# Kernel optimization log

Measured on AMD Instinct MI355X. Metric: run time of the kernel, lower is better.

Reference implementation:

```python
import jax, jax.numpy as jnp
import numpy as np


def setup_inputs() -> dict:
    key = jax.random.key(0)
    k1, k2 = jax.random.split(key)
    N, P, D = 65536, 512, 256
    feature_vectors = jax.random.normal(k1, (N, D), dtype=jnp.float32)
    prototypes = jax.random.normal(k2, (P, D), dtype=jnp.float32)
    return {"feature_vectors": feature_vectors, "prototypes": prototypes}


def reference(feature_vectors, prototypes):
    # squared norms
    feat_sq = jnp.sum(feature_vectors * feature_vectors, axis=1)   # [N]
    proto_sq = jnp.sum(prototypes * prototypes, axis=1)            # [P]
    # cross term: [N, P]
    cross = feature_vectors @ prototypes.T
    # dists_to_protos: [N, P] = |f|^2 + |p|^2 - 2 f.p
    dists_to_protos = feat_sq[:, None] + proto_sq[None, :] - 2.0 * cross
    # dists_to_latents: [P, N] (original does a second matmul; it's the transpose)
    dists_to_latents = proto_sq[:, None] + feat_sq[None, :] - 2.0 * cross.T
    return (dists_to_protos, dists_to_latents)
```

## Files before the change

### kernel.cpp

```cpp
#include <hip/hip_runtime.h>
#include <hip/hip_bf16.h>


#define DD 256
#define PP 512
#define BN 64
#define TP 36

typedef short bf16x8 __attribute__((ext_vector_type(8)));
typedef float f32x16 __attribute__((ext_vector_type(16)));
typedef float f32x4 __attribute__((ext_vector_type(4)));
typedef unsigned short u16x4 __attribute__((ext_vector_type(4)));

__device__ __forceinline__ unsigned short f2bf(float f) {
    unsigned int u = __builtin_bit_cast(unsigned int, f);
    u = (u + 0x7fffu + ((u >> 16) & 1u)) >> 16;
    return (unsigned short)u;
}

__global__ __launch_bounds__(256) void proto_prep(const float* __restrict__ proto,
                                                  unsigned short* __restrict__ bw,
                                                  float* __restrict__ psq) {
    const int w = threadIdx.x >> 6, lane = threadIdx.x & 63;
    const int row = blockIdx.x * 4 + w;
    const f32x4 f = *(const f32x4*)(proto + (size_t)row * DD + lane * 4);
    u16x4 u;
    u.x = f2bf(f.x); u.y = f2bf(f.y); u.z = f2bf(f.z); u.w = f2bf(f.w);
    *(u16x4*)(bw + (size_t)row * DD + lane * 4) = u;
    float part = f.x * f.x + f.y * f.y + f.z * f.z + f.w * f.w;
    for (int o = 32; o > 0; o >>= 1) part += __shfl_xor(part, o, 64);
    if (lane == 0) psq[row] = part;
}

__global__ __launch_bounds__(512, 4) void proto_dist(
        const float* __restrict__ feat,
        const unsigned short* __restrict__ bw,
        const float* __restrict__ psq,
        float* __restrict__ out0,
        float* __restrict__ out1,
        int N) {
    __shared__ unsigned char S[8 * 32 * TP * 4];
    __shared__ float fsq[BN];
    unsigned short* A_lds = (unsigned short*)S;

    const int tid = threadIdx.x;
    const int w = tid >> 6, lane = tid & 63;
    const int n0 = blockIdx.x * BN;

    #pragma unroll
    for (int i = 0; i < 8; ++i) {
        const int row = i * 8 + w;
        const f32x4 f = __builtin_nontemporal_load(
            (const f32x4*)(feat + (size_t)(n0 + row) * DD + lane * 4));
        u16x4 u;
        u.x = f2bf(f.x); u.y = f2bf(f.y); u.z = f2bf(f.z); u.w = f2bf(f.w);
        *(u16x4*)&A_lds[row * 264 + lane * 4] = u;
        float part = f.x * f.x + f.y * f.y + f.z * f.z + f.w * f.w;
        for (int o = 32; o > 0; o >>= 1) part += __shfl_xor(part, o, 64);
        if (lane == 0) fsq[row] = part;
    }
    __syncthreads();

    const int r = w & 1;
    const int g = w >> 1;
    const int colbase = g * 128;
    const int l31 = lane & 31;
    const int hi = lane >> 5;

    f32x16 acc[4];
    #pragma unroll
    for (int t = 0; t < 4; ++t)
        #pragma unroll
        for (int e = 0; e < 16; ++e) acc[t][e] = 0.0f;

    const unsigned short* arow = &A_lds[(32 * r + l31) * 264 + hi * 8];
    const unsigned short* bbase = bw + (size_t)(colbase + l31) * DD + hi * 8;

    #pragma unroll 2
    for (int k0 = 0; k0 < DD; k0 += 16) {
        const bf16x8 a = *(const bf16x8*)(arow + k0);
        #pragma unroll
        for (int t = 0; t < 4; ++t) {
            const bf16x8 b = *(const bf16x8*)(bbase + (size_t)(32 * t) * DD + k0);
            acc[t] = __builtin_amdgcn_mfma_f32_32x32x16_bf16(a, b, acc[t], 0, 0, 0);
        }
    }

    __syncthreads();
    float* trans = ((float*)S) + w * (32 * TP);

    float fsq_q[4][4];
    #pragma unroll
    for (int q = 0; q < 4; ++q)
        #pragma unroll
        for (int e = 0; e < 4; ++e)
            fsq_q[q][e] = fsq[32 * r + e + 8 * q + 4 * hi];

    float* out0_base = out0 + (size_t)(n0 + 32 * r) * PP;

    #pragma unroll
    for (int t = 0; t < 4; ++t) {
        const int p = colbase + 32 * t + l31;
        const float psq_v = psq[p];
        #pragma unroll
        for (int q = 0; q < 4; ++q) {
            f32x4 d;
            #pragma unroll
            for (int e = 0; e < 4; ++e) {
                const int reg = 4 * q + e;
                const int n_l = e + 8 * q + 4 * hi;
                const float dist = fsq_q[q][e] + psq_v - 2.0f * acc[t][reg];
                d[e] = dist;
                __builtin_nontemporal_store(dist, out0_base + (size_t)n_l * PP + p);
            }
            *(f32x4*)&trans[l31 * TP + 8 * q + 4 * hi] = d;
        }
        #pragma unroll
        for (int j = 0; j < 4; ++j) {
            const int p_row = j * 8 + (lane >> 3);
            const int n_off = (lane & 7) * 4;
            const f32x4 v = *(const f32x4*)&trans[p_row * TP + n_off];
            __builtin_nontemporal_store(v,
                (f32x4*)(out1 + (size_t)(colbase + 32 * t + p_row) * N
                               + (n0 + 32 * r + n_off)));
        }
    }
}

extern "C" void kernel_launch(void* const* d_in, const int* in_sizes, int n_in,
                              void* d_out, int out_size, void* d_ws, size_t ws_size,
                              hipStream_t stream) {
    const float* feat = (const float*)d_in[0];
    const float* proto = (const float*)d_in[1];
    const int N = in_sizes[0] / DD;

    unsigned short* bw = (unsigned short*)d_ws;
    float* psq = (float*)((char*)d_ws + (size_t)PP * DD * 2);

    float* out0 = (float*)d_out;
    float* out1 = out0 + (size_t)N * PP;

    proto_prep<<<PP / 4, 256, 0, stream>>>(proto, bw, psq);
    proto_dist<<<N / BN, 512, 0, stream>>>(feat, bw, psq, out0, out1, N);
}
```

Measured before the change: 357.3 us.

## Load features straight from global into MFMA operands, dropping the LDS staging

The block tile shrinks from 64 to 32 feature rows with 4 waves instead of 8. Each wave now reads its fp32 feature slice from global memory inside the k-loop, converts it to bf16 in registers and accumulates the squared norm, with a lane shuffle replacing the shared fsq array. This removes the LDS staging pass and one barrier, and gives more, smaller blocks. In exchange, every wave in a block re-reads the same feature rows from global/cache (4x redundancy), and the strided per-lane loads are less coalesced.

After: 385.3 us. 7.8% more time.

```diff
diff --git a/kernel.cpp b/kernel.cpp
--- a/kernel.cpp
+++ b/kernel.cpp
@@ -4,7 +4,7 @@
 
 #define DD 256
 #define PP 512
-#define BN 64
+#define BN 32
 #define TP 36
 
 typedef short bf16x8 __attribute__((ext_vector_type(8)));
@@ -32,40 +32,24 @@
     if (lane == 0) psq[row] = part;
 }
 
-__global__ __launch_bounds__(512, 4) void proto_dist(
+__global__ __launch_bounds__(256, 4) void proto_dist(
         const float* __restrict__ feat,
         const unsigned short* __restrict__ bw,
         const float* __restrict__ psq,
         float* __restrict__ out0,
         float* __restrict__ out1,
         int N) {
-    __shared__ unsigned char S[8 * 32 * TP * 4];
-    __shared__ float fsq[BN];
-    unsigned short* A_lds = (unsigned short*)S;
+    __shared__ float S[4 * 32 * TP];
 
     const int tid = threadIdx.x;
     const int w = tid >> 6, lane = tid & 63;
     const int n0 = blockIdx.x * BN;
-
-    #pragma unroll
-    for (int i = 0; i < 8; ++i) {
-        const int row = i * 8 + w;
-        const f32x4 f = __builtin_nontemporal_load(
-            (const f32x4*)(feat + (size_t)(n0 + row) * DD + lane * 4));
-        u16x4 u;
-        u.x = f2bf(f.x); u.y = f2bf(f.y); u.z = f2bf(f.z); u.w = f2bf(f.w);
-        *(u16x4*)&A_lds[row * 264 + lane * 4] = u;
-        float part = f.x * f.x + f.y * f.y + f.z * f.z + f.w * f.w;
-        for (int o = 32; o > 0; o >>= 1) part += __shfl_xor(part, o, 64);
-        if (lane == 0) fsq[row] = part;
-    }
-    __syncthreads();
-
-    const int r = w & 1;
-    const int g = w >> 1;
-    const int colbase = g * 128;
+    const int colbase = w * 128;
     const int l31 = lane & 31;
     const int hi = lane >> 5;
+
+    const float* arow = feat + (size_t)(n0 + l31) * DD + hi * 8;
+    const unsigned short* bbase = bw + (size_t)(colbase + l31) * DD + hi * 8;
 
     f32x16 acc[4];
     #pragma unroll
@@ -73,12 +57,19 @@
         #pragma unroll
         for (int e = 0; e < 16; ++e) acc[t][e] = 0.0f;
 
-    const unsigned short* arow = &A_lds[(32 * r + l31) * 264 + hi * 8];
-    const unsigned short* bbase = bw + (size_t)(colbase + l31) * DD + hi * 8;
+    float part = 0.0f;
 
     #pragma unroll 2
     for (int k0 = 0; k0 < DD; k0 += 16) {
-        const bf16x8 a = *(const bf16x8*)(arow + k0);
+        const f32x4 f0 = *(const f32x4*)(arow + k0);
+        const f32x4 f1 = *(const f32x4*)(arow + k0 + 4);
+        bf16x8 a;
+        a[0] = (short)f2bf(f0.x); a[1] = (short)f2bf(f0.y);
+        a[2] = (short)f2bf(f0.z); a[3] = (short)f2bf(f0.w);
+        a[4] = (short)f2bf(f1.x); a[5] = (short)f2bf(f1.y);
+        a[6] = (short)f2bf(f1.z); a[7] = (short)f2bf(f1.w);
+        part += f0.x * f0.x + f0.y * f0.y + f0.z * f0.z + f0.w * f0.w
+              + f1.x * f1.x + f1.y * f1.y + f1.z * f1.z + f1.w * f1.w;
         #pragma unroll
         for (int t = 0; t < 4; ++t) {
             const bf16x8 b = *(const bf16x8*)(bbase + (size_t)(32 * t) * DD + k0);
@@ -86,17 +77,16 @@
         }
     }
 
-    __syncthreads();
-    float* trans = ((float*)S) + w * (32 * TP);
-
+    part += __shfl_xor(part, 32, 64);
     float fsq_q[4][4];
     #pragma unroll
     for (int q = 0; q < 4; ++q)
         #pragma unroll
         for (int e = 0; e < 4; ++e)
-            fsq_q[q][e] = fsq[32 * r + e + 8 * q + 4 * hi];
+            fsq_q[q][e] = __shfl(part, e + 8 * q + 4 * hi, 64);
 
-    float* out0_base = out0 + (size_t)(n0 + 32 * r) * PP;
+    float* trans = S + w * (32 * TP);
+    float* out0_base = out0 + (size_t)n0 * PP;
 
     #pragma unroll
     for (int t = 0; t < 4; ++t) {
@@ -122,7 +112,7 @@
             const f32x4 v = *(const f32x4*)&trans[p_row * TP + n_off];
             __builtin_nontemporal_store(v,
                 (f32x4*)(out1 + (size_t)(colbase + 32 * t + p_row) * N
-                               + (n0 + 32 * r + n_off)));
+                               + (n0 + n_off)));
         }
     }
 }
@@ -141,5 +131,5 @@
     float* out1 = out0 + (size_t)N * PP;
 
     proto_prep<<<PP / 4, 256, 0, stream>>>(proto, bw, psq);
-    proto_dist<<<N / BN, 512, 0, stream>>>(feat, bw, psq, out0, out1, N);
+    proto_dist<<<N / BN, 256, 0, stream>>>(feat, bw, psq, out0, out1, N);
 }
```

## Compute transposed output via second swapped MFMA instead of LDS transpose

Applied to the files above, without the earlier changes.

Replaces the LDS-based transpose of the cross-term tile with a second MFMA that uses swapped operands, so the transposed tile for the second output comes straight out of the accumulators. The block tile shrinks to 32 feature rows with 256 threads, and each wave loops over its four 32-column prototype tiles with fresh accumulators. This removes the shared-memory round trip and a barrier, but doubles the MFMA work. The second output is now written as scalar stores of 32 consecutive floats per row (128 bytes) rather than f32x4 vector stores. Prototype fragments are reread from global memory by twice as many blocks.

After: 376.0 us. 5.2% more time.

```diff
diff --git a/kernel.cpp b/kernel.cpp
--- a/kernel.cpp
+++ b/kernel.cpp
@@ -4,8 +4,8 @@
 
 #define DD 256
 #define PP 512
-#define BN 64
-#define TP 36
+#define BN 32
+#define AP 280
 
 typedef short bf16x8 __attribute__((ext_vector_type(8)));
 typedef float f32x16 __attribute__((ext_vector_type(16)));
@@ -32,16 +32,15 @@
     if (lane == 0) psq[row] = part;
 }
 
-__global__ __launch_bounds__(512, 4) void proto_dist(
+__global__ __launch_bounds__(256, 4) void proto_dist(
         const float* __restrict__ feat,
         const unsigned short* __restrict__ bw,
         const float* __restrict__ psq,
         float* __restrict__ out0,
         float* __restrict__ out1,
         int N) {
-    __shared__ unsigned char S[8 * 32 * TP * 4];
+    __shared__ unsigned short A_lds[BN * AP];
     __shared__ float fsq[BN];
-    unsigned short* A_lds = (unsigned short*)S;
 
     const int tid = threadIdx.x;
     const int w = tid >> 6, lane = tid & 63;
@@ -49,80 +48,69 @@
 
     #pragma unroll
     for (int i = 0; i < 8; ++i) {
-        const int row = i * 8 + w;
+        const int row = i * 4 + w;
         const f32x4 f = __builtin_nontemporal_load(
             (const f32x4*)(feat + (size_t)(n0 + row) * DD + lane * 4));
         u16x4 u;
         u.x = f2bf(f.x); u.y = f2bf(f.y); u.z = f2bf(f.z); u.w = f2bf(f.w);
-        *(u16x4*)&A_lds[row * 264 + lane * 4] = u;
+        *(u16x4*)&A_lds[row * AP + lane * 4] = u;
         float part = f.x * f.x + f.y * f.y + f.z * f.z + f.w * f.w;
         for (int o = 32; o > 0; o >>= 1) part += __shfl_xor(part, o, 64);
         if (lane == 0) fsq[row] = part;
     }
     __syncthreads();
 
-    const int r = w & 1;
-    const int g = w >> 1;
-    const int colbase = g * 128;
     const int l31 = lane & 31;
     const int hi = lane >> 5;
+    const int colT = w * 128;
 
-    f32x16 acc[4];
-    #pragma unroll
-    for (int t = 0; t < 4; ++t)
-        #pragma unroll
-        for (int e = 0; e < 16; ++e) acc[t][e] = 0.0f;
+    const unsigned short* arow = &A_lds[l31 * AP + hi * 8];
 
-    const unsigned short* arow = &A_lds[(32 * r + l31) * 264 + hi * 8];
-    const unsigned short* bbase = bw + (size_t)(colbase + l31) * DD + hi * 8;
-
-    #pragma unroll 2
-    for (int k0 = 0; k0 < DD; k0 += 16) {
-        const bf16x8 a = *(const bf16x8*)(arow + k0);
-        #pragma unroll
-        for (int t = 0; t < 4; ++t) {
-            const bf16x8 b = *(const bf16x8*)(bbase + (size_t)(32 * t) * DD + k0);
-            acc[t] = __builtin_amdgcn_mfma_f32_32x32x16_bf16(a, b, acc[t], 0, 0, 0);
-        }
-    }
-
-    __syncthreads();
-    float* trans = ((float*)S) + w * (32 * TP);
-
-    float fsq_q[4][4];
+    f32x4 fsq_q[4];
     #pragma unroll
     for (int q = 0; q < 4; ++q)
-        #pragma unroll
-        for (int e = 0; e < 4; ++e)
-            fsq_q[q][e] = fsq[32 * r + e + 8 * q + 4 * hi];
-
-    float* out0_base = out0 + (size_t)(n0 + 32 * r) * PP;
+        fsq_q[q] = *(const f32x4*)&fsq[8 * q + 4 * hi];
+    const float fsq_lane = fsq[l31];
 
     #pragma unroll
     for (int t = 0; t < 4; ++t) {
-        const int p = colbase + 32 * t + l31;
-        const float psq_v = psq[p];
+        const int pbase = colT + 32 * t;
+        const unsigned short* bb = bw + (size_t)(pbase + l31) * DD + hi * 8;
+
+        f32x16 acc, acc2;
+        #pragma unroll
+        for (int e = 0; e < 16; ++e) { acc[e] = 0.0f; acc2[e] = 0.0f; }
+
+        #pragma unroll 4
+        for (int k0 = 0; k0 < DD; k0 += 16) {
+            const bf16x8 a = *(const bf16x8*)(arow + k0);
+            const bf16x8 b = *(const bf16x8*)(bb + k0);
+            acc  = __builtin_amdgcn_mfma_f32_32x32x16_bf16(a, b, acc,  0, 0, 0);
+            acc2 = __builtin_amdgcn_mfma_f32_32x32x16_bf16(b, a, acc2, 0, 0, 0);
+        }
+
+        const float psq_lane = psq[pbase + l31];
+        float* o0 = out0 + (size_t)n0 * PP + pbase + l31;
         #pragma unroll
         for (int q = 0; q < 4; ++q) {
-            f32x4 d;
             #pragma unroll
             for (int e = 0; e < 4; ++e) {
-                const int reg = 4 * q + e;
                 const int n_l = e + 8 * q + 4 * hi;
-                const float dist = fsq_q[q][e] + psq_v - 2.0f * acc[t][reg];
-                d[e] = dist;
-                __builtin_nontemporal_store(dist, out0_base + (size_t)n_l * PP + p);
+                const float dist = fsq_q[q][e] + psq_lane - 2.0f * acc[4 * q + e];
+                __builtin_nontemporal_store(dist, o0 + (size_t)n_l * PP);
             }
-            *(f32x4*)&trans[l31 * TP + 8 * q + 4 * hi] = d;
         }
+
+        float* o1 = out1 + (size_t)pbase * N + n0 + l31;
         #pragma unroll
-        for (int j = 0; j < 4; ++j) {
-            const int p_row = j * 8 + (lane >> 3);
-            const int n_off = (lane & 7) * 4;
-            const f32x4 v = *(const f32x4*)&trans[p_row * TP + n_off];
-            __builtin_nontemporal_store(v,
-                (f32x4*)(out1 + (size_t)(colbase + 32 * t + p_row) * N
-                               + (n0 + 32 * r + n_off)));
+        for (int q = 0; q < 4; ++q) {
+            const f32x4 ps4 = *(const f32x4*)(psq + pbase + 8 * q + 4 * hi);
+            #pragma unroll
+            for (int e = 0; e < 4; ++e) {
+                const int p_l = e + 8 * q + 4 * hi;
+                const float dist = fsq_lane + ps4[e] - 2.0f * acc2[4 * q + e];
+                __builtin_nontemporal_store(dist, o1 + (size_t)p_l * N);
+            }
         }
     }
 }
@@ -141,5 +129,5 @@
     float* out1 = out0 + (size_t)N * PP;
 
     proto_prep<<<PP / 4, 256, 0, stream>>>(proto, bw, psq);
-    proto_dist<<<N / BN, 512, 0, stream>>>(feat, bw, psq, out0, out1, N);
+    proto_dist<<<N / BN, 256, 0, stream>>>(feat, bw, psq, out0, out1, N);
 }
```

## Stage both outputs through block-wide LDS tiles for fully coalesced vector stores

Applied to the files above, without the earlier changes.

Replaces the per-wave scalar out0 stores and the 32-wide transposed out1 stores with block-wide staging. Each output is written in phases: 32 rows x 512 columns for out0, and 128 prototypes x 64 features for out1, each followed by 16-byte nontemporal stores of whole contiguous rows. The goal is to remove uncoalesced scalar writes to out0 and short segments to out1 on this store-bound kernel. In exchange, LDS grows to 64KB, which limits occupancy, and it adds about ten block barriers that serialise waves during the epilogue.

After: 359.2 us. Within noise of the previous version (+0.5%).

```diff
diff --git a/kernel.cpp b/kernel.cpp
--- a/kernel.cpp
+++ b/kernel.cpp
@@ -5,7 +5,8 @@
 #define DD 256
 #define PP 512
 #define BN 64
-#define TP 36
+#define AP 280
+#define O1S 68
 
 typedef short bf16x8 __attribute__((ext_vector_type(8)));
 typedef float f32x16 __attribute__((ext_vector_type(16)));
@@ -39,9 +40,10 @@
         float* __restrict__ out0,
         float* __restrict__ out1,
         int N) {
-    __shared__ unsigned char S[8 * 32 * TP * 4];
+    __shared__ unsigned char S[65536];
     __shared__ float fsq[BN];
     unsigned short* A_lds = (unsigned short*)S;
+    float* lds_f = (float*)S;
 
     const int tid = threadIdx.x;
     const int w = tid >> 6, lane = tid & 63;
@@ -54,7 +56,7 @@
             (const f32x4*)(feat + (size_t)(n0 + row) * DD + lane * 4));
         u16x4 u;
         u.x = f2bf(f.x); u.y = f2bf(f.y); u.z = f2bf(f.z); u.w = f2bf(f.w);
-        *(u16x4*)&A_lds[row * 264 + lane * 4] = u;
+        *(u16x4*)&A_lds[row * AP + lane * 4] = u;
         float part = f.x * f.x + f.y * f.y + f.z * f.z + f.w * f.w;
         for (int o = 32; o > 0; o >>= 1) part += __shfl_xor(part, o, 64);
         if (lane == 0) fsq[row] = part;
@@ -63,9 +65,11 @@
 
     const int r = w & 1;
     const int g = w >> 1;
-    const int colbase = g * 128;
+    const int colT = g * 128;
     const int l31 = lane & 31;
     const int hi = lane >> 5;
+
+    const unsigned short* arow = &A_lds[(32 * r + l31) * AP + hi * 8];
 
     f32x16 acc[4];
     #pragma unroll
@@ -73,57 +77,81 @@
         #pragma unroll
         for (int e = 0; e < 16; ++e) acc[t][e] = 0.0f;
 
-    const unsigned short* arow = &A_lds[(32 * r + l31) * 264 + hi * 8];
-    const unsigned short* bbase = bw + (size_t)(colbase + l31) * DD + hi * 8;
-
     #pragma unroll 2
     for (int k0 = 0; k0 < DD; k0 += 16) {
         const bf16x8 a = *(const bf16x8*)(arow + k0);
         #pragma unroll
         for (int t = 0; t < 4; ++t) {
-            const bf16x8 b = *(const bf16x8*)(bbase + (size_t)(32 * t) * DD + k0);
+            const bf16x8 b = *(const bf16x8*)(
+                bw + (size_t)(colT + 32 * t + l31) * DD + hi * 8 + k0);
             acc[t] = __builtin_amdgcn_mfma_f32_32x32x16_bf16(a, b, acc[t], 0, 0, 0);
         }
     }
 
-    __syncthreads();
-    float* trans = ((float*)S) + w * (32 * TP);
-
-    float fsq_q[4][4];
+    f32x4 fsq_q[4];
     #pragma unroll
     for (int q = 0; q < 4; ++q)
-        #pragma unroll
-        for (int e = 0; e < 4; ++e)
-            fsq_q[q][e] = fsq[32 * r + e + 8 * q + 4 * hi];
+        fsq_q[q] = *(const f32x4*)&fsq[32 * r + 8 * q + 4 * hi];
+    f32x4 psqv;
+    #pragma unroll
+    for (int t = 0; t < 4; ++t) psqv[t] = psq[colT + 32 * t + l31];
 
-    float* out0_base = out0 + (size_t)(n0 + 32 * r) * PP;
+    __syncthreads();
 
     #pragma unroll
-    for (int t = 0; t < 4; ++t) {
-        const int p = colbase + 32 * t + l31;
-        const float psq_v = psq[p];
+    for (int s = 0; s < 2; ++s) {
+        if (r == s) {
+            #pragma unroll
+            for (int t = 0; t < 4; ++t)
+                #pragma unroll
+                for (int q = 0; q < 4; ++q)
+                    #pragma unroll
+                    for (int e = 0; e < 4; ++e) {
+                        const int n_l = e + 8 * q + 4 * hi;
+                        lds_f[n_l * 512 + colT + 32 * t + l31] =
+                            fsq_q[q][e] + psqv[t] - 2.0f * acc[t][4 * q + e];
+                    }
+        }
+        __syncthreads();
+        float* o0 = out0 + (size_t)(n0 + 32 * s) * PP;
+        const int row = tid >> 7;
+        const int off = (tid & 127) * 4;
         #pragma unroll
-        for (int q = 0; q < 4; ++q) {
-            f32x4 d;
+        for (int rr = 0; rr < 8; ++rr) {
+            const f32x4 v = *(const f32x4*)&lds_f[(row + 4 * rr) * 512 + off];
+            __builtin_nontemporal_store(
+                v, (f32x4*)(o0 + (size_t)(row + 4 * rr) * PP + off));
+        }
+        __syncthreads();
+    }
+
+    #pragma unroll
+    for (int sp = 0; sp < 4; ++sp) {
+        if (g == sp) {
             #pragma unroll
-            for (int e = 0; e < 4; ++e) {
-                const int reg = 4 * q + e;
-                const int n_l = e + 8 * q + 4 * hi;
-                const float dist = fsq_q[q][e] + psq_v - 2.0f * acc[t][reg];
-                d[e] = dist;
-                __builtin_nontemporal_store(dist, out0_base + (size_t)n_l * PP + p);
+            for (int t = 0; t < 4; ++t) {
+                const int p_loc = 32 * t + l31;
+                #pragma unroll
+                for (int q = 0; q < 4; ++q) {
+                    f32x4 d;
+                    #pragma unroll
+                    for (int e = 0; e < 4; ++e)
+                        d[e] = fsq_q[q][e] + psqv[t] - 2.0f * acc[t][4 * q + e];
+                    *(f32x4*)&lds_f[p_loc * O1S + 32 * r + 8 * q + 4 * hi] = d;
+                }
             }
-            *(f32x4*)&trans[l31 * TP + 8 * q + 4 * hi] = d;
         }
+        __syncthreads();
+        const int p_row = tid >> 4;
+        const int n_off = (tid & 15) * 4;
+        float* o1 = out1 + (size_t)(128 * sp) * N + n0;
         #pragma unroll
-        for (int j = 0; j < 4; ++j) {
-            const int p_row = j * 8 + (lane >> 3);
-            const int n_off = (lane & 7) * 4;
-            const f32x4 v = *(const f32x4*)&trans[p_row * TP + n_off];
-            __builtin_nontemporal_store(v,
-                (f32x4*)(out1 + (size_t)(colbase + 32 * t + p_row) * N
-                               + (n0 + 32 * r + n_off)));
+        for (int rr = 0; rr < 4; ++rr) {
+            const f32x4 v = *(const f32x4*)&lds_f[(p_row + 32 * rr) * O1S + n_off];
+            __builtin_nontemporal_store(
+                v, (f32x4*)(o1 + (size_t)(p_row + 32 * rr) * N + n_off));
         }
+        if (sp < 3) __syncthreads();
     }
 }
 
```
